# Kernel tuning notes

Hardware: AMD Instinct MI355X
Metric: run time of the kernel (lower is better)

## Reference

```python
import jax, jax.numpy as jnp
import numpy as np

N = 20000
E = 320000
IN_DIM, HID, MID, OUT, HEADS = 1536, 512, 128, 5, 8
NEG_SLOPE = 0.2
BN_EPS = 1e-5


def gat_conv(x, edge_index, W, a_src, a_dst, bias, heads, out_ch):
    """PyG-style GATConv (eval mode, self-loops already in edge_index).
    x: [N, F_in]; W: [F_in, heads*out_ch]; a_src/a_dst: [heads, out_ch]; bias: [heads*out_ch].
    Returns [N, heads*out_ch] (head concat)."""
    n = x.shape[0]
    h = (x @ W).reshape(n, heads, out_ch)              # [N,H,C]
    src, dst = edge_index[0], edge_index[1]
    al_s = jnp.sum(h * a_src, axis=-1)                 # [N,H]
    al_d = jnp.sum(h * a_dst, axis=-1)                 # [N,H]
    e = al_s[src] + al_d[dst]                          # [E,H]
    e = jnp.where(e >= 0, e, NEG_SLOPE * e)            # leaky_relu
    # segment softmax over incoming edges per dst node
    e_max = jax.ops.segment_max(e, dst, num_segments=n)
    e_max = jnp.where(jnp.isfinite(e_max), e_max, 0.0)
    ex = jnp.exp(e - e_max[dst])                       # [E,H]
    denom = jax.ops.segment_sum(ex, dst, num_segments=n)
    alpha = ex / (denom[dst] + 1e-16)                  # [E,H]
    msg = h[src] * alpha[:, :, None]                   # [E,H,C]
    out = jax.ops.segment_sum(msg, dst, num_segments=n)
    return out.reshape(n, heads * out_ch) + bias


def bn_eval(x, gamma, beta, mean, var):
    return (x - mean) * jax.lax.rsqrt(var + BN_EPS) * gamma + beta


def setup_inputs() -> dict:
    key = jax.random.key(0)
    ks = jax.random.split(key, 24)
    x = jax.random.normal(ks[0], (N, IN_DIM), dtype=jnp.float32)
    edge_index = jax.random.randint(ks[1], (2, E), 0, N, dtype=jnp.int32)

    def glorot(k, shape):
        fan = shape[0] + shape[-1]
        return jax.random.normal(k, shape, dtype=jnp.float32) * np.sqrt(2.0 / fan)

    inp = {"x": x, "edge_index": edge_index}
    # conv1: 1536 -> 8 heads x 64
    inp["W1"] = glorot(ks[2], (IN_DIM, HID))
    inp["as1"] = glorot(ks[3], (HEADS, HID // HEADS))
    inp["ad1"] = glorot(ks[4], (HEADS, HID // HEADS))
    inp["b1"] = jnp.zeros((HID,), jnp.float32)
    # conv2: 512 -> 8 heads x 16
    inp["W2"] = glorot(ks[5], (HID, MID))
    inp["as2"] = glorot(ks[6], (HEADS, MID // HEADS))
    inp["ad2"] = glorot(ks[7], (HEADS, MID // HEADS))
    inp["b2"] = jnp.zeros((MID,), jnp.float32)
    # conv3: 128 -> 1 head x 5
    inp["W3"] = glorot(ks[8], (MID, OUT))
    inp["as3"] = glorot(ks[9], (1, OUT))
    inp["ad3"] = glorot(ks[10], (1, OUT))
    inp["b3"] = jnp.zeros((OUT,), jnp.float32)
    # batchnorm params (eval mode, running stats)
    inp["g1"] = jax.random.normal(ks[11], (HID,), jnp.float32) * 0.1 + 1.0
    inp["be1"] = jax.random.normal(ks[12], (HID,), jnp.float32) * 0.1
    inp["m1"] = jax.random.normal(ks[13], (HID,), jnp.float32) * 0.1
    inp["v1"] = jax.random.uniform(ks[14], (HID,), jnp.float32, 0.5, 1.5)
    inp["g2"] = jax.random.normal(ks[15], (MID,), jnp.float32) * 0.1 + 1.0
    inp["be2"] = jax.random.normal(ks[16], (MID,), jnp.float32) * 0.1
    inp["m2"] = jax.random.normal(ks[17], (MID,), jnp.float32) * 0.1
    inp["v2"] = jax.random.uniform(ks[18], (MID,), jnp.float32, 0.5, 1.5)
    return inp


def reference(x, edge_index, W1, as1, ad1, b1, W2, as2, ad2, b2, W3, as3, ad3, b3,
              g1, be1, m1, v1, g2, be2, m2, v2):
    # add self-loops (PyG GATConv default)
    loops = jnp.arange(N, dtype=edge_index.dtype)
    ei = jnp.concatenate([edge_index, jnp.stack([loops, loops])], axis=1)

    h = jax.nn.relu(gat_conv(x, ei, W1, as1, ad1, b1, HEADS, HID // HEADS))
    h = bn_eval(h, g1, be1, m1, v1)
    h = jax.nn.relu(gat_conv(h, ei, W2, as2, ad2, b2, HEADS, MID // HEADS))
    h = bn_eval(h, g2, be2, m2, v2)
    h = gat_conv(h, ei, W3, as3, ad3, b3, 1, OUT)
    return jax.nn.log_softmax(h, axis=1)
```

## Files before the change

### kernel.cpp

```cpp
#include <hip/hip_runtime.h>
#include <math.h>

#define IN_DIM 1536
#define HID 512
#define MID 128
#define OUTC 5
#define HEADS 8
#define NEG_SLOPE 0.2f
#define BN_EPS 1e-5f

typedef __attribute__((ext_vector_type(8))) short s16x8;
typedef __attribute__((ext_vector_type(4))) float fx4;

__device__ __forceinline__ unsigned short bf16_rne(float f) {
    unsigned int u = __float_as_uint(f);
    u += 0x7fffu + ((u >> 16) & 1u);
    return (unsigned short)(u >> 16);
}
__device__ __forceinline__ float bf16_to_f32(unsigned short u) {
    return __uint_as_float((unsigned int)u << 16);
}

__device__ __forceinline__ void async_copy16(void* lds, const void* g) {
    __builtin_amdgcn_global_load_lds(
        (const __attribute__((address_space(1))) unsigned int*)g,
        (__attribute__((address_space(3))) unsigned int*)lds, 16, 0, 0);
}

__global__ void hist_kernel(const int* __restrict__ ei, int* __restrict__ deg,
                            int ET, int E) {
    int e = blockIdx.x * blockDim.x + threadIdx.x;
    if (e >= ET) return;
    int dst = (e < E) ? ei[E + e] : (e - E);
    atomicAdd(&deg[dst], 1);
}

__global__ __launch_bounds__(1024) void scan_kernel(const int* __restrict__ deg,
                                                    int* __restrict__ row_ptr,
                                                    int* __restrict__ cursor, int n) {
    __shared__ int partial[1024];
    int tid = threadIdx.x;
    int per = (n + 1023) / 1024;
    int base = tid * per;
    int s = 0;
    for (int i = 0; i < per; ++i) {
        int idx = base + i;
        if (idx < n) s += deg[idx];
    }
    partial[tid] = s;
    __syncthreads();
    for (int off = 1; off < 1024; off <<= 1) {
        int v = (tid >= off) ? partial[tid - off] : 0;
        __syncthreads();
        partial[tid] += v;
        __syncthreads();
    }
    int prefix = (tid == 0) ? 0 : partial[tid - 1];
    for (int i = 0; i < per; ++i) {
        int idx = base + i;
        if (idx < n) {
            row_ptr[idx] = prefix;
            cursor[idx] = prefix;
            prefix += deg[idx];
        }
    }
    if (tid == 1023) row_ptr[n] = partial[1023];
}

__global__ void scatter_kernel(const int* __restrict__ ei, int* __restrict__ cursor,
                               int* __restrict__ csr_src, int ET, int E) {
    int e = blockIdx.x * blockDim.x + threadIdx.x;
    if (e >= ET) return;
    int src, dst;
    if (e < E) { src = ei[e]; dst = ei[E + e]; }
    else       { src = dst = e - E; }
    int slot = atomicAdd(&cursor[dst], 1);
    csr_src[slot] = src;
}

__global__ void cvt_bf16_kernel(const float* __restrict__ in,
                                unsigned short* __restrict__ out, int n4) {
    int i = blockIdx.x * blockDim.x + threadIdx.x;
    if (i >= n4) return;
    float4 v = ((const float4*)in)[i];
    ushort4 o;
    o.x = bf16_rne(v.x); o.y = bf16_rne(v.y);
    o.z = bf16_rne(v.z); o.w = bf16_rne(v.w);
    ((ushort4*)out)[i] = o;
}

template <bool WLO>
__global__ __launch_bounds__(256) void transpose_split(
    const float* __restrict__ W, unsigned short* __restrict__ Th,
    unsigned short* __restrict__ Tl, int K, int Nn) {
    __shared__ float tile[32][33];
    int kb = blockIdx.y * 32, nb = blockIdx.x * 32;
    int tx = threadIdx.x & 31, ty = threadIdx.x >> 5;
#pragma unroll
    for (int r = 0; r < 4; ++r)
        tile[ty + r * 8][tx] = W[(size_t)(kb + ty + r * 8) * Nn + nb + tx];
    __syncthreads();
#pragma unroll
    for (int r = 0; r < 4; ++r) {
        int n = ty + r * 8;
        float v = tile[tx][n];
        unsigned short hi = bf16_rne(v);
        size_t o = (size_t)(nb + n) * K + kb + tx;
        Th[o] = hi;
        if (WLO) {
            float hif = __uint_as_float((unsigned int)hi << 16);
            Tl[o] = bf16_rne(v - hif);
        }
    }
}

__global__ __launch_bounds__(256) void gemm1_kernel(
    const unsigned short* __restrict__ A, const unsigned short* __restrict__ Bh,
    unsigned short* __restrict__ Cb, const float* __restrict__ a_s,
    const float* __restrict__ a_d, float* __restrict__ als,
    float* __restrict__ ald, int M, int N, int K, int MBLK) {
    int b = blockIdx.x;
    int xm = (b & 7) + 8 * (b >> 5);
    int ym = (b >> 3) & 3;
    if (xm >= MBLK) return;

    __shared__ unsigned short Asb[2][128 * 32];
    __shared__ unsigned short Bsb[2][128 * 32];

    const int tid = threadIdx.x;
    const int lane = tid & 63;
    const int wv = tid >> 6;
    const int row0 = xm * 128;
    const int nb0 = ym * 128;
    const int col = lane & 15;
    const int quad = lane >> 4;
    const int m0 = (wv >> 1) * 64;
    const int n0 = (wv & 1) * 64;

    const int s_row = lane >> 2;
    const int s_chunk = (lane & 3) ^ ((lane >> 3) & 3);
    int agr0 = row0 + (wv * 2 + 0) * 16 + s_row; if (agr0 >= M) agr0 = M - 1;
    int agr1 = row0 + (wv * 2 + 1) * 16 + s_row; if (agr1 >= M) agr1 = M - 1;
    const size_t ag0 = (size_t)agr0 * K + s_chunk * 8;
    const size_t ag1 = (size_t)agr1 * K + s_chunk * 8;
    const size_t bg0 = (size_t)(nb0 + (wv * 2 + 0) * 16 + s_row) * K + s_chunk * 8;
    const size_t bg1 = (size_t)(nb0 + (wv * 2 + 1) * 16 + s_row) * K + s_chunk * 8;

    const int rsw = (col >> 1) & 3;

    fx4 acc[4][4];
#pragma unroll
    for (int i = 0; i < 4; ++i)
#pragma unroll
        for (int j = 0; j < 4; ++j) acc[i][j] = (fx4){0.f, 0.f, 0.f, 0.f};

    async_copy16(&Asb[0][(wv * 2 + 0) * 512], A + ag0);
    async_copy16(&Asb[0][(wv * 2 + 1) * 512], A + ag1);
    async_copy16(&Bsb[0][(wv * 2 + 0) * 512], Bh + bg0);
    async_copy16(&Bsb[0][(wv * 2 + 1) * 512], Bh + bg1);
    __syncthreads();

    int cur = 0;
    for (int k0 = 0; k0 < K; k0 += 32) {
        const int nxt = cur ^ 1;
        if (k0 + 32 < K) {
            const int kn = k0 + 32;
            async_copy16(&Asb[nxt][(wv * 2 + 0) * 512], A + ag0 + kn);
            async_copy16(&Asb[nxt][(wv * 2 + 1) * 512], A + ag1 + kn);
            async_copy16(&Bsb[nxt][(wv * 2 + 0) * 512], Bh + bg0 + kn);
            async_copy16(&Bsb[nxt][(wv * 2 + 1) * 512], Bh + bg1 + kn);
        }
        s16x8 afr[4], bfr[4];
#pragma unroll
        for (int i = 0; i < 4; ++i)
            afr[i] = *(const s16x8*)&Asb[cur][(m0 + i * 16 + col) * 32 + (quad ^ rsw) * 8];
#pragma unroll
        for (int j = 0; j < 4; ++j)
            bfr[j] = *(const s16x8*)&Bsb[cur][(n0 + j * 16 + col) * 32 + (quad ^ rsw) * 8];
#pragma unroll
        for (int i = 0; i < 4; ++i)
#pragma unroll
            for (int j = 0; j < 4; ++j)
                acc[i][j] = __builtin_amdgcn_mfma_f32_16x16x32_bf16(afr[i], bfr[j], acc[i][j], 0, 0, 0);
        __syncthreads();
        cur = nxt;
    }

#pragma unroll
    for (int i = 0; i < 4; ++i) {
        int gr0 = row0 + m0 + i * 16 + quad * 4;
#pragma unroll
        for (int j = 0; j < 4; ++j) {
            int gc = nb0 + n0 + j * 16 + col;
#pragma unroll
            for (int r = 0; r < 4; ++r) {
                int gr = gr0 + r;
                if (gr < M) Cb[(size_t)gr * N + gc] = bf16_rne(acc[i][j][r]);
            }
        }
    }

    const int head = (nb0 + n0) >> 6;
    float asv[4], adv[4];
#pragma unroll
    for (int j = 0; j < 4; ++j) {
        asv[j] = a_s[head * 64 + j * 16 + col];
        adv[j] = a_d[head * 64 + j * 16 + col];
    }
#pragma unroll
    for (int i = 0; i < 4; ++i) {
#pragma unroll
        for (int r = 0; r < 4; ++r) {
            float ss = acc[i][0][r] * asv[0] + acc[i][1][r] * asv[1] +
                       acc[i][2][r] * asv[2] + acc[i][3][r] * asv[3];
            float sd = acc[i][0][r] * adv[0] + acc[i][1][r] * adv[1] +
                       acc[i][2][r] * adv[2] + acc[i][3][r] * adv[3];
#pragma unroll
            for (int off = 8; off; off >>= 1) {
                ss += __shfl_xor(ss, off);
                sd += __shfl_xor(sd, off);
            }
            if (col == 0) {
                int gr = row0 + m0 + i * 16 + quad * 4 + r;
                if (gr < M) {
                    als[gr * HEADS + head] = ss;
                    ald[gr * HEADS + head] = sd;
                }
            }
        }
    }
}

__global__ __launch_bounds__(256) void gemm2_kernel(
    const unsigned short* __restrict__ A, const unsigned short* __restrict__ Bh,
    const unsigned short* __restrict__ Bl, unsigned short* __restrict__ Cb,
    const float* __restrict__ a_s, const float* __restrict__ a_d,
    float* __restrict__ als, float* __restrict__ ald, int M, int N, int K) {
    __shared__ unsigned short Asb[2][32 * 32];
    __shared__ unsigned short Bhb[2][128 * 32];
    __shared__ unsigned short Blb[2][128 * 32];

    const int tid = threadIdx.x;
    const int lane = tid & 63;
    const int wv = tid >> 6;
    const int row0 = blockIdx.x * 32;
    const int col = lane & 15;
    const int quad = lane >> 4;
    const int m0 = (wv >> 1) * 16;
    const int n0 = (wv & 1) * 64;
    const int b_row = lane >> 2;
    const int b_chunk = (lane & 3) ^ ((lane >> 3) & 3);
    const int rsw = (col >> 1) & 3;

    const int t0 = wv * 2, t1 = t0 + 1;
    const size_t bgo0 = (size_t)(t0 * 16 + b_row) * K + b_chunk * 8;
    const size_t bgo1 = (size_t)(t1 * 16 + b_row) * K + b_chunk * 8;
    int agr = row0 + wv * 16 + b_row; if (agr >= M) agr = M - 1;
    const size_t ago = (size_t)agr * K + b_chunk * 8;

    fx4 acc[4];
#pragma unroll
    for (int j = 0; j < 4; ++j) acc[j] = (fx4){0.f, 0.f, 0.f, 0.f};

    auto stage = [&](int buf, int k) {
        async_copy16(&Bhb[buf][t0 * 512], Bh + bgo0 + k);
        async_copy16(&Bhb[buf][t1 * 512], Bh + bgo1 + k);
        async_copy16(&Blb[buf][t0 * 512], Bl + bgo0 + k);
        async_copy16(&Blb[buf][t1 * 512], Bl + bgo1 + k);
        if (wv < 2) async_copy16(&Asb[buf][wv * 512], A + ago + k);
    };

    stage(0, 0);
    __syncthreads();

    int cur = 0;
    for (int k0 = 0; k0 < K; k0 += 32) {
        const int nxt = cur ^ 1;
        if (k0 + 32 < K) stage(nxt, k0 + 32);
        s16x8 a, bh4[4], bl4[4];
        a = *(const s16x8*)&Asb[cur][(m0 + col) * 32 + (quad ^ rsw) * 8];
#pragma unroll
        for (int j = 0; j < 4; ++j) {
            int rb = (n0 + j * 16 + col) * 32 + (quad ^ rsw) * 8;
            bh4[j] = *(const s16x8*)&Bhb[cur][rb];
            bl4[j] = *(const s16x8*)&Blb[cur][rb];
        }
#pragma unroll
        for (int j = 0; j < 4; ++j) {
            acc[j] = __builtin_amdgcn_mfma_f32_16x16x32_bf16(a, bl4[j], acc[j], 0, 0, 0);
            acc[j] = __builtin_amdgcn_mfma_f32_16x16x32_bf16(a, bh4[j], acc[j], 0, 0, 0);
        }
        __syncthreads();
        cur = nxt;
    }

    int gr0 = row0 + m0 + quad * 4;
#pragma unroll
    for (int j = 0; j < 4; ++j) {
        int gc = n0 + j * 16 + col;
#pragma unroll
        for (int r = 0; r < 4; ++r) {
            int gr = gr0 + r;
            if (gr < M) Cb[(size_t)gr * N + gc] = bf16_rne(acc[j][r]);
        }
    }

    float asv[4], adv[4];
#pragma unroll
    for (int j = 0; j < 4; ++j) {
        asv[j] = a_s[n0 + j * 16 + col];
        adv[j] = a_d[n0 + j * 16 + col];
    }
#pragma unroll
    for (int j = 0; j < 4; ++j) {
        int head = (n0 >> 4) + j;
#pragma unroll
        for (int r = 0; r < 4; ++r) {
            float ss = acc[j][r] * asv[j];
            float sd = acc[j][r] * adv[j];
#pragma unroll
            for (int off = 8; off; off >>= 1) {
                ss += __shfl_xor(ss, off);
                sd += __shfl_xor(sd, off);
            }
            if (col == 0) {
                int gr = gr0 + r;
                if (gr < M) {
                    als[gr * HEADS + head] = ss;
                    ald[gr * HEADS + head] = sd;
                }
            }
        }
    }
}

template <int F, int VEC>
__global__ __launch_bounds__(128) void agg_fused_kernel(
    const unsigned short* __restrict__ hlin, const float* __restrict__ als,
    const float* __restrict__ ald, const int* __restrict__ row_ptr,
    const int* __restrict__ csr_src, const float* __restrict__ bias,
    const float* __restrict__ gamma, const float* __restrict__ beta,
    const float* __restrict__ mean, const float* __restrict__ var,
    unsigned short* __restrict__ outh) {
    int dst = blockIdx.x;
    int tid = threadIdx.x;
    int f0 = tid * VEC;
    int h = tid >> 4;
    __shared__ float exs[16][8];
    __shared__ int srcs[16];
    int s0 = row_ptr[dst], s1 = row_ptr[dst + 1];
    int cj = tid >> 3, ch = tid & 7;
    float ald_c = ald[dst * HEADS + ch];
    float acc[VEC];
#pragma unroll
    for (int v = 0; v < VEC; ++v) acc[v] = 0.f;
    float den = 0.f;

    for (int base = s0; base < s1; base += 16) {
        int take = min(16, s1 - base);
        if (cj < take) {
            int src = csr_src[base + cj];
            if (ch == 0) srcs[cj] = src;
            float e = als[src * HEADS + ch] + ald_c;
            e = (e >= 0.f) ? e : NEG_SLOPE * e;
            exs[cj][ch] = __expf(e);
        }
        __syncthreads();
        for (int jj = 0; jj < take; ++jj) {
            int src = srcs[jj];
            float a = exs[jj][h];
            den += a;
            const unsigned short* rp = &hlin[(size_t)src * F + f0];
            ushort4 u = *(const ushort4*)rp;
            acc[0] += a * bf16_to_f32(u.x);
            acc[1] += a * bf16_to_f32(u.y);
            acc[2] += a * bf16_to_f32(u.z);
            acc[3] += a * bf16_to_f32(u.w);
        }
        __syncthreads();
    }

    float rd = 1.f / (den + 1e-16f);
    ushort4 o;
    unsigned short* op = (unsigned short*)&o;
#pragma unroll
    for (int v = 0; v < VEC; ++v) {
        int f = f0 + v;
        float val = acc[v] * rd + bias[f];
        val = fmaxf(val, 0.f);
        val = (val - mean[f]) * rsqrtf(var[f] + BN_EPS) * gamma[f] + beta[f];
        op[v] = bf16_rne(val);
    }
    *(ushort4*)&outh[(size_t)dst * F + f0] = o;
}

__global__ __launch_bounds__(128) void agg2_l3_kernel(
    const unsigned short* __restrict__ hlin, const float* __restrict__ als,
    const float* __restrict__ ald, const int* __restrict__ row_ptr,
    const int* __restrict__ csr_src, const float* __restrict__ bias,
    const float* __restrict__ gamma, const float* __restrict__ beta,
    const float* __restrict__ mean, const float* __restrict__ var,
    const float* __restrict__ W3, const float* __restrict__ as3,
    const float* __restrict__ ad3, float* __restrict__ h3lin,
    float* __restrict__ als3, float* __restrict__ ald3) {
    int dst = blockIdx.x;
    int tid = threadIdx.x;
    int h = tid >> 4;
    __shared__ float exs[16][8];
    __shared__ int srcs[16];
    __shared__ float red[2][OUTC];
    int s0 = row_ptr[dst], s1 = row_ptr[dst + 1];
    int cj = tid >> 3, ch = tid & 7;
    float ald_c = ald[dst * HEADS + ch];
    float acc = 0.f, den = 0.f;

    for (int base = s0; base < s1; base += 16) {
        int take = min(16, s1 - base);
        if (cj < take) {
            int src = csr_src[base + cj];
            if (ch == 0) srcs[cj] = src;
            float e = als[src * HEADS + ch] + ald_c;
            e = (e >= 0.f) ? e : NEG_SLOPE * e;
            exs[cj][ch] = __expf(e);
        }
        __syncthreads();
        for (int jj = 0; jj < take; ++jj) {
            int src = srcs[jj];
            float a = exs[jj][h];
            den += a;
            acc += a * bf16_to_f32(hlin[(size_t)src * MID + tid]);
        }
        __syncthreads();
    }

    float val = acc / (den + 1e-16f) + bias[tid];
    val = fmaxf(val, 0.f);
    val = (val - mean[tid]) * rsqrtf(var[tid] + BN_EPS) * gamma[tid] + beta[tid];

    float p[OUTC];
#pragma unroll
    for (int c = 0; c < OUTC; ++c) p[c] = val * W3[tid * OUTC + c];
#pragma unroll
    for (int off = 32; off; off >>= 1) {
#pragma unroll
        for (int c = 0; c < OUTC; ++c) p[c] += __shfl_xor(p[c], off);
    }
    int wv = tid >> 6;
    if ((tid & 63) == 0) {
#pragma unroll
        for (int c = 0; c < OUTC; ++c) red[wv][c] = p[c];
    }
    __syncthreads();
    if (tid == 0) {
        float ss = 0.f, sd = 0.f;
#pragma unroll
        for (int c = 0; c < OUTC; ++c) {
            float v = red[0][c] + red[1][c];
            h3lin[(size_t)dst * OUTC + c] = v;
            ss += v * as3[c];
            sd += v * ad3[c];
        }
        als3[dst] = ss;
        ald3[dst] = sd;
    }
}

__global__ __launch_bounds__(256) void agg3_lsm_kernel(
    const float* __restrict__ h3lin, const float* __restrict__ als,
    const float* __restrict__ ald, const int* __restrict__ row_ptr,
    const int* __restrict__ csr_src, const float* __restrict__ b3,
    float* __restrict__ out, int n) {
    int g = blockIdx.x * blockDim.x + threadIdx.x;
    int dst = g >> 4;
    int l = g & 15;
    if (dst >= n) return;
    int s0 = row_ptr[dst], s1 = row_ptr[dst + 1];
    float ad = ald[dst];
    float den = 0.f;
    float acc[OUTC] = {0.f, 0.f, 0.f, 0.f, 0.f};
    for (int j = s0 + l; j < s1; j += 16) {
        int src = csr_src[j];
        float e = als[src] + ad;
        e = (e >= 0.f) ? e : NEG_SLOPE * e;
        float x = __expf(e);
        den += x;
        const float* hp = h3lin + (size_t)src * OUTC;
#pragma unroll
        for (int c = 0; c < OUTC; ++c) acc[c] += x * hp[c];
    }
#pragma unroll
    for (int off = 8; off; off >>= 1) {
        den += __shfl_xor(den, off);
#pragma unroll
        for (int c = 0; c < OUTC; ++c) acc[c] += __shfl_xor(acc[c], off);
    }
    if (l == 0) {
        float rd = 1.f / (den + 1e-16f);
        float m = -INFINITY;
#pragma unroll
        for (int c = 0; c < OUTC; ++c) {
            acc[c] = acc[c] * rd + b3[c];
            m = fmaxf(m, acc[c]);
        }
        float s = 0.f;
#pragma unroll
        for (int c = 0; c < OUTC; ++c) s += __expf(acc[c] - m);
        float lse = m + __logf(s);
#pragma unroll
        for (int c = 0; c < OUTC; ++c) out[(size_t)dst * OUTC + c] = acc[c] - lse;
    }
}

extern "C" void kernel_launch(void* const* d_in, const int* in_sizes, int n_in,
                              void* d_out, int out_size, void* d_ws, size_t ws_size,
                              hipStream_t stream) {
    const float* x   = (const float*)d_in[0];
    const int*   ei  = (const int*)d_in[1];
    const float* W1  = (const float*)d_in[2];
    const float* as1 = (const float*)d_in[3];
    const float* ad1 = (const float*)d_in[4];
    const float* b1  = (const float*)d_in[5];
    const float* W2  = (const float*)d_in[6];
    const float* as2 = (const float*)d_in[7];
    const float* ad2 = (const float*)d_in[8];
    const float* b2  = (const float*)d_in[9];
    const float* W3  = (const float*)d_in[10];
    const float* as3 = (const float*)d_in[11];
    const float* ad3 = (const float*)d_in[12];
    const float* b3  = (const float*)d_in[13];
    const float* g1  = (const float*)d_in[14];
    const float* be1 = (const float*)d_in[15];
    const float* m1  = (const float*)d_in[16];
    const float* v1  = (const float*)d_in[17];
    const float* g2  = (const float*)d_in[18];
    const float* be2 = (const float*)d_in[19];
    const float* m2  = (const float*)d_in[20];
    const float* v2  = (const float*)d_in[21];

    const int N = in_sizes[0] / IN_DIM;
    const int E = in_sizes[1] / 2;
    const int ET = E + N;
    const int MBLK1 = (N + 127) / 128;
    const int MBLK2 = (N + 31) / 32;

    char* ws = (char*)d_ws;
    size_t off = 0;
    auto take = [&](size_t bytes) -> char* {
        char* p = ws + off;
        off += (bytes + 255) & ~(size_t)255;
        return p;
    };
    int* deg      = (int*)take((size_t)N * 4);
    int* row_ptr  = (int*)take((size_t)(N + 1) * 4);
    int* cursor   = (int*)take((size_t)N * 4);
    int* csr_src  = (int*)take((size_t)ET * 4);
    unsigned short* W1h = (unsigned short*)take((size_t)HID * IN_DIM * 2);
    unsigned short* W2h = (unsigned short*)take((size_t)MID * HID * 2);
    unsigned short* W2l = (unsigned short*)take((size_t)MID * HID * 2);
    unsigned short* xh  = (unsigned short*)take((size_t)N * IN_DIM * 2);
    unsigned short* h1lin = (unsigned short*)take((size_t)N * HID * 2);
    unsigned short* h1h   = (unsigned short*)take((size_t)N * HID * 2);
    unsigned short* h2lin = (unsigned short*)take((size_t)N * MID * 2);
    float* h3lin  = (float*)take((size_t)N * OUTC * 4);
    float* als    = (float*)take((size_t)N * HEADS * 4);
    float* ald    = (float*)take((size_t)N * HEADS * 4);
    float* als3   = (float*)take((size_t)N * 4);
    float* ald3   = (float*)take((size_t)N * 4);

    hipMemsetAsync(deg, 0, (size_t)N * 4, stream);
    hist_kernel<<<(ET + 255) / 256, 256, 0, stream>>>(ei, deg, ET, E);
    scan_kernel<<<1, 1024, 0, stream>>>(deg, row_ptr, cursor, N);
    scatter_kernel<<<(ET + 255) / 256, 256, 0, stream>>>(ei, cursor, csr_src, ET, E);
    transpose_split<false><<<dim3(HID / 32, IN_DIM / 32), 256, 0, stream>>>(
        W1, W1h, nullptr, IN_DIM, HID);
    transpose_split<true><<<dim3(MID / 32, HID / 32), 256, 0, stream>>>(
        W2, W2h, W2l, HID, MID);
    {
        int n4 = N * IN_DIM / 4;
        cvt_bf16_kernel<<<(n4 + 255) / 256, 256, 0, stream>>>(x, xh, n4);
    }

    gemm1_kernel<<<640, 256, 0, stream>>>(xh, W1h, h1lin, as1, ad1, als, ald,
                                          N, HID, IN_DIM, MBLK1);
    agg_fused_kernel<HID, 4><<<N, 128, 0, stream>>>(
        h1lin, als, ald, row_ptr, csr_src, b1, g1, be1, m1, v1, h1h);

    gemm2_kernel<<<MBLK2, 256, 0, stream>>>(h1h, W2h, W2l, h2lin, as2, ad2,
                                            als, ald, N, MID, HID);
    agg2_l3_kernel<<<N, 128, 0, stream>>>(
        h2lin, als, ald, row_ptr, csr_src, b2, g2, be2, m2, v2,
        W3, as3, ad3, h3lin, als3, ald3);

    agg3_lsm_kernel<<<(N * 16 + 255) / 256, 256, 0, stream>>>(
        h3lin, als3, ald3, row_ptr, csr_src, b3, (float*)d_out, N);
}
```

Measured before the change: 446.0 us.

## Fuse fp32-to-bf16 conversion of x into gemm1 tile loads and merge transposes

Removes the standalone conversion kernel and the bf16 copy of x. gemm1 now loads fp32 rows of x into registers, converts them, and writes the bf16 tile to LDS after the MFMA work for software pipelining. The two weight transpose launches are merged into one kernel. The trade is losing async LDS copies for A and having each N-block reread fp32 data, which doubles the per-tile read bytes.

Measured after the change: 474.1 us. +6.3%, slower.

```diff
diff --git a/kernel.cpp b/kernel.cpp
--- a/kernel.cpp
+++ b/kernel.cpp
@@ -25,6 +25,15 @@
     __builtin_amdgcn_global_load_lds(
         (const __attribute__((address_space(1))) unsigned int*)g,
         (__attribute__((address_space(3))) unsigned int*)lds, 16, 0, 0);
+}
+
+__device__ __forceinline__ void store_bf16x8(unsigned short* p, float4 a, float4 b) {
+    union { s16x8 v; unsigned short u[8]; } o;
+    o.u[0] = bf16_rne(a.x); o.u[1] = bf16_rne(a.y);
+    o.u[2] = bf16_rne(a.z); o.u[3] = bf16_rne(a.w);
+    o.u[4] = bf16_rne(b.x); o.u[5] = bf16_rne(b.y);
+    o.u[6] = bf16_rne(b.z); o.u[7] = bf16_rne(b.w);
+    *(s16x8*)p = o.v;
 }
 
 __global__ void hist_kernel(const int* __restrict__ ei, int* __restrict__ deg,
@@ -78,23 +87,24 @@
     csr_src[slot] = src;
 }
 
-__global__ void cvt_bf16_kernel(const float* __restrict__ in,
-                                unsigned short* __restrict__ out, int n4) {
-    int i = blockIdx.x * blockDim.x + threadIdx.x;
-    if (i >= n4) return;
-    float4 v = ((const float4*)in)[i];
-    ushort4 o;
-    o.x = bf16_rne(v.x); o.y = bf16_rne(v.y);
-    o.z = bf16_rne(v.z); o.w = bf16_rne(v.w);
-    ((ushort4*)out)[i] = o;
-}
-
-template <bool WLO>
-__global__ __launch_bounds__(256) void transpose_split(
-    const float* __restrict__ W, unsigned short* __restrict__ Th,
-    unsigned short* __restrict__ Tl, int K, int Nn) {
+__global__ __launch_bounds__(256) void transpose_both_kernel(
+    const float* __restrict__ W1, unsigned short* __restrict__ W1h,
+    const float* __restrict__ W2, unsigned short* __restrict__ W2h,
+    unsigned short* __restrict__ W2l) {
     __shared__ float tile[32][33];
-    int kb = blockIdx.y * 32, nb = blockIdx.x * 32;
+    int b = blockIdx.x;
+    const float* W;
+    unsigned short *Th, *Tl;
+    int K, Nn, kb, nb;
+    bool wlo;
+    if (b < 768) {
+        W = W1; Th = W1h; Tl = nullptr; wlo = false; K = IN_DIM; Nn = HID;
+        nb = (b & 15) * 32; kb = (b >> 4) * 32;
+    } else {
+        int b2 = b - 768;
+        W = W2; Th = W2h; Tl = W2l; wlo = true; K = HID; Nn = MID;
+        nb = (b2 & 3) * 32; kb = (b2 >> 2) * 32;
+    }
     int tx = threadIdx.x & 31, ty = threadIdx.x >> 5;
 #pragma unroll
     for (int r = 0; r < 4; ++r)
@@ -107,7 +117,7 @@
         unsigned short hi = bf16_rne(v);
         size_t o = (size_t)(nb + n) * K + kb + tx;
         Th[o] = hi;
-        if (WLO) {
+        if (wlo) {
             float hif = __uint_as_float((unsigned int)hi << 16);
             Tl[o] = bf16_rne(v - hif);
         }
@@ -115,7 +125,7 @@
 }
 
 __global__ __launch_bounds__(256) void gemm1_kernel(
-    const unsigned short* __restrict__ A, const unsigned short* __restrict__ Bh,
+    const float* __restrict__ Af, const unsigned short* __restrict__ Bh,
     unsigned short* __restrict__ Cb, const float* __restrict__ a_s,
     const float* __restrict__ a_d, float* __restrict__ als,
     float* __restrict__ ald, int M, int N, int K, int MBLK) {
@@ -137,12 +147,18 @@
     const int m0 = (wv >> 1) * 64;
     const int n0 = (wv & 1) * 64;
 
+    const int ar0 = tid >> 2;
+    const int ac = tid & 3;
+    const int ag = ac ^ ((ar0 >> 1) & 3);
+    int arow0 = row0 + ar0;      if (arow0 >= M) arow0 = M - 1;
+    int arow1 = row0 + ar0 + 64; if (arow1 >= M) arow1 = M - 1;
+    const size_t aoff0 = (size_t)arow0 * K + ag * 8;
+    const size_t aoff1 = (size_t)arow1 * K + ag * 8;
+    const int lds_a0 = ar0 * 32 + ac * 8;
+    const int lds_a1 = (ar0 + 64) * 32 + ac * 8;
+
     const int s_row = lane >> 2;
     const int s_chunk = (lane & 3) ^ ((lane >> 3) & 3);
-    int agr0 = row0 + (wv * 2 + 0) * 16 + s_row; if (agr0 >= M) agr0 = M - 1;
-    int agr1 = row0 + (wv * 2 + 1) * 16 + s_row; if (agr1 >= M) agr1 = M - 1;
-    const size_t ag0 = (size_t)agr0 * K + s_chunk * 8;
-    const size_t ag1 = (size_t)agr1 * K + s_chunk * 8;
     const size_t bg0 = (size_t)(nb0 + (wv * 2 + 0) * 16 + s_row) * K + s_chunk * 8;
     const size_t bg1 = (size_t)(nb0 + (wv * 2 + 1) * 16 + s_row) * K + s_chunk * 8;
 
@@ -154,19 +170,29 @@
 #pragma unroll
         for (int j = 0; j < 4; ++j) acc[i][j] = (fx4){0.f, 0.f, 0.f, 0.f};
 
-    async_copy16(&Asb[0][(wv * 2 + 0) * 512], A + ag0);
-    async_copy16(&Asb[0][(wv * 2 + 1) * 512], A + ag1);
-    async_copy16(&Bsb[0][(wv * 2 + 0) * 512], Bh + bg0);
-    async_copy16(&Bsb[0][(wv * 2 + 1) * 512], Bh + bg1);
+    {
+        float4 p00 = *(const float4*)(Af + aoff0);
+        float4 p01 = *(const float4*)(Af + aoff0 + 4);
+        float4 p10 = *(const float4*)(Af + aoff1);
+        float4 p11 = *(const float4*)(Af + aoff1 + 4);
+        async_copy16(&Bsb[0][(wv * 2 + 0) * 512], Bh + bg0);
+        async_copy16(&Bsb[0][(wv * 2 + 1) * 512], Bh + bg1);
+        store_bf16x8(&Asb[0][lds_a0], p00, p01);
+        store_bf16x8(&Asb[0][lds_a1], p10, p11);
+    }
     __syncthreads();
 
     int cur = 0;
     for (int k0 = 0; k0 < K; k0 += 32) {
         const int nxt = cur ^ 1;
-        if (k0 + 32 < K) {
+        const bool more = (k0 + 32 < K);
+        float4 p00, p01, p10, p11;
+        if (more) {
             const int kn = k0 + 32;
-            async_copy16(&Asb[nxt][(wv * 2 + 0) * 512], A + ag0 + kn);
-            async_copy16(&Asb[nxt][(wv * 2 + 1) * 512], A + ag1 + kn);
+            p00 = *(const float4*)(Af + aoff0 + kn);
+            p01 = *(const float4*)(Af + aoff0 + kn + 4);
+            p10 = *(const float4*)(Af + aoff1 + kn);
+            p11 = *(const float4*)(Af + aoff1 + kn + 4);
             async_copy16(&Bsb[nxt][(wv * 2 + 0) * 512], Bh + bg0 + kn);
             async_copy16(&Bsb[nxt][(wv * 2 + 1) * 512], Bh + bg1 + kn);
         }
@@ -182,6 +208,10 @@
 #pragma unroll
             for (int j = 0; j < 4; ++j)
                 acc[i][j] = __builtin_amdgcn_mfma_f32_16x16x32_bf16(afr[i], bfr[j], acc[i][j], 0, 0, 0);
+        if (more) {
+            store_bf16x8(&Asb[nxt][lds_a0], p00, p01);
+            store_bf16x8(&Asb[nxt][lds_a1], p10, p11);
+        }
         __syncthreads();
         cur = nxt;
     }
@@ -557,7 +587,6 @@
     unsigned short* W1h = (unsigned short*)take((size_t)HID * IN_DIM * 2);
     unsigned short* W2h = (unsigned short*)take((size_t)MID * HID * 2);
     unsigned short* W2l = (unsigned short*)take((size_t)MID * HID * 2);
-    unsigned short* xh  = (unsigned short*)take((size_t)N * IN_DIM * 2);
     unsigned short* h1lin = (unsigned short*)take((size_t)N * HID * 2);
     unsigned short* h1h   = (unsigned short*)take((size_t)N * HID * 2);
     unsigned short* h2lin = (unsigned short*)take((size_t)N * MID * 2);
@@ -571,16 +600,9 @@
     hist_kernel<<<(ET + 255) / 256, 256, 0, stream>>>(ei, deg, ET, E);
     scan_kernel<<<1, 1024, 0, stream>>>(deg, row_ptr, cursor, N);
     scatter_kernel<<<(ET + 255) / 256, 256, 0, stream>>>(ei, cursor, csr_src, ET, E);
-    transpose_split<false><<<dim3(HID / 32, IN_DIM / 32), 256, 0, stream>>>(
-        W1, W1h, nullptr, IN_DIM, HID);
-    transpose_split<true><<<dim3(MID / 32, HID / 32), 256, 0, stream>>>(
-        W2, W2h, W2l, HID, MID);
-    {
-        int n4 = N * IN_DIM / 4;
-        cvt_bf16_kernel<<<(n4 + 255) / 256, 256, 0, stream>>>(x, xh, n4);
-    }
-
-    gemm1_kernel<<<640, 256, 0, stream>>>(xh, W1h, h1lin, as1, ad1, als, ald,
+    transpose_both_kernel<<<832, 256, 0, stream>>>(W1, W1h, W2, W2h, W2l);
+
+    gemm1_kernel<<<640, 256, 0, stream>>>(x, W1h, h1lin, as1, ad1, als, ald,
                                           N, HID, IN_DIM, MBLK1);
     agg_fused_kernel<HID, 4><<<N, 128, 0, stream>>>(
         h1lin, als, ald, row_ptr, csr_src, b1, g1, be1, m1, v1, h1h);
```

## Use one wavefront per node in layer-1 aggregation and merge weight transposes

Applied to the files above, without the earlier changes.

Layer-1 aggregation now runs one 64-lane wavefront per destination node with four nodes per block. Attention weights and source indices are passed between lanes with shuffles, so the shared memory and block barriers are gone. Each lane loads 8 bf16 features at once in a single 16-byte access. The two weight-transpose launches are merged into one kernel to save a launch, at the cost of handling only 8 edges per chunk instead of 16.

Result: no change. 446.7 us (+0.2%).

```diff
diff --git a/kernel.cpp b/kernel.cpp
--- a/kernel.cpp
+++ b/kernel.cpp
@@ -89,12 +89,24 @@
     ((ushort4*)out)[i] = o;
 }
 
-template <bool WLO>
-__global__ __launch_bounds__(256) void transpose_split(
-    const float* __restrict__ W, unsigned short* __restrict__ Th,
-    unsigned short* __restrict__ Tl, int K, int Nn) {
+__global__ __launch_bounds__(256) void transpose_both_kernel(
+    const float* __restrict__ W1, unsigned short* __restrict__ W1h,
+    const float* __restrict__ W2, unsigned short* __restrict__ W2h,
+    unsigned short* __restrict__ W2l) {
     __shared__ float tile[32][33];
-    int kb = blockIdx.y * 32, nb = blockIdx.x * 32;
+    int b = blockIdx.x;
+    const float* W;
+    unsigned short *Th, *Tl;
+    int K, Nn, kb, nb;
+    bool wlo;
+    if (b < 768) {
+        W = W1; Th = W1h; Tl = nullptr; wlo = false; K = IN_DIM; Nn = HID;
+        nb = (b & 15) * 32; kb = (b >> 4) * 32;
+    } else {
+        int b2 = b - 768;
+        W = W2; Th = W2h; Tl = W2l; wlo = true; K = HID; Nn = MID;
+        nb = (b2 & 3) * 32; kb = (b2 >> 2) * 32;
+    }
     int tx = threadIdx.x & 31, ty = threadIdx.x >> 5;
 #pragma unroll
     for (int r = 0; r < 4; ++r)
@@ -107,7 +119,7 @@
         unsigned short hi = bf16_rne(v);
         size_t o = (size_t)(nb + n) * K + kb + tx;
         Th[o] = hi;
-        if (WLO) {
+        if (wlo) {
             float hif = __uint_as_float((unsigned int)hi << 16);
             Tl[o] = bf16_rne(v - hif);
         }
@@ -334,64 +346,60 @@
     }
 }
 
-template <int F, int VEC>
-__global__ __launch_bounds__(128) void agg_fused_kernel(
+__global__ __launch_bounds__(256) void agg1_wave_kernel(
     const unsigned short* __restrict__ hlin, const float* __restrict__ als,
     const float* __restrict__ ald, const int* __restrict__ row_ptr,
     const int* __restrict__ csr_src, const float* __restrict__ bias,
     const float* __restrict__ gamma, const float* __restrict__ beta,
     const float* __restrict__ mean, const float* __restrict__ var,
-    unsigned short* __restrict__ outh) {
-    int dst = blockIdx.x;
-    int tid = threadIdx.x;
-    int f0 = tid * VEC;
-    int h = tid >> 4;
-    __shared__ float exs[16][8];
-    __shared__ int srcs[16];
+    unsigned short* __restrict__ outh, int n) {
+    int lane = threadIdx.x & 63;
+    int dst = blockIdx.x * 4 + (threadIdx.x >> 6);
+    if (dst >= n) return;
+    const int f0 = lane * 8;
+    const int h = lane >> 3;
+    const int j8 = lane >> 3;
+    const int ch = lane & 7;
+    float ald_c = ald[dst * HEADS + ch];
+
     int s0 = row_ptr[dst], s1 = row_ptr[dst + 1];
-    int cj = tid >> 3, ch = tid & 7;
-    float ald_c = ald[dst * HEADS + ch];
-    float acc[VEC];
-#pragma unroll
-    for (int v = 0; v < VEC; ++v) acc[v] = 0.f;
+    float acc[8];
+#pragma unroll
+    for (int v = 0; v < 8; ++v) acc[v] = 0.f;
     float den = 0.f;
 
-    for (int base = s0; base < s1; base += 16) {
-        int take = min(16, s1 - base);
-        if (cj < take) {
-            int src = csr_src[base + cj];
-            if (ch == 0) srcs[cj] = src;
-            float e = als[src * HEADS + ch] + ald_c;
+    for (int base = s0; base < s1; base += 8) {
+        int take = min(8, s1 - base);
+        float ex = 0.f;
+        int src_l = 0;
+        if (j8 < take) {
+            src_l = csr_src[base + j8];
+            float e = als[src_l * HEADS + ch] + ald_c;
             e = (e >= 0.f) ? e : NEG_SLOPE * e;
-            exs[cj][ch] = __expf(e);
-        }
-        __syncthreads();
+            ex = __expf(e);
+        }
         for (int jj = 0; jj < take; ++jj) {
-            int src = srcs[jj];
-            float a = exs[jj][h];
+            int src = __shfl(src_l, jj * 8);
+            float a = __shfl(ex, jj * 8 + h);
             den += a;
-            const unsigned short* rp = &hlin[(size_t)src * F + f0];
-            ushort4 u = *(const ushort4*)rp;
-            acc[0] += a * bf16_to_f32(u.x);
-            acc[1] += a * bf16_to_f32(u.y);
-            acc[2] += a * bf16_to_f32(u.z);
-            acc[3] += a * bf16_to_f32(u.w);
-        }
-        __syncthreads();
+            union { s16x8 v; unsigned short u[8]; } w;
+            w.v = *(const s16x8*)&hlin[(size_t)src * HID + f0];
+#pragma unroll
+            for (int v = 0; v < 8; ++v) acc[v] += a * bf16_to_f32(w.u[v]);
+        }
     }
 
     float rd = 1.f / (den + 1e-16f);
-    ushort4 o;
-    unsigned short* op = (unsigned short*)&o;
-#pragma unroll
-    for (int v = 0; v < VEC; ++v) {
+    union { s16x8 v; unsigned short u[8]; } o;
+#pragma unroll
+    for (int v = 0; v < 8; ++v) {
         int f = f0 + v;
         float val = acc[v] * rd + bias[f];
         val = fmaxf(val, 0.f);
         val = (val - mean[f]) * rsqrtf(var[f] + BN_EPS) * gamma[f] + beta[f];
-        op[v] = bf16_rne(val);
-    }
-    *(ushort4*)&outh[(size_t)dst * F + f0] = o;
+        o.u[v] = bf16_rne(val);
+    }
+    *(s16x8*)&outh[(size_t)dst * HID + f0] = o.v;
 }
 
 __global__ __launch_bounds__(128) void agg2_l3_kernel(
@@ -571,10 +579,7 @@
     hist_kernel<<<(ET + 255) / 256, 256, 0, stream>>>(ei, deg, ET, E);
     scan_kernel<<<1, 1024, 0, stream>>>(deg, row_ptr, cursor, N);
     scatter_kernel<<<(ET + 255) / 256, 256, 0, stream>>>(ei, cursor, csr_src, ET, E);
-    transpose_split<false><<<dim3(HID / 32, IN_DIM / 32), 256, 0, stream>>>(
-        W1, W1h, nullptr, IN_DIM, HID);
-    transpose_split<true><<<dim3(MID / 32, HID / 32), 256, 0, stream>>>(
-        W2, W2h, W2l, HID, MID);
+    transpose_both_kernel<<<832, 256, 0, stream>>>(W1, W1h, W2, W2h, W2l);
     {
         int n4 = N * IN_DIM / 4;
         cvt_bf16_kernel<<<(n4 + 255) / 256, 256, 0, stream>>>(x, xh, n4);
@@ -582,8 +587,8 @@
 
     gemm1_kernel<<<640, 256, 0, stream>>>(xh, W1h, h1lin, as1, ad1, als, ald,
                                           N, HID, IN_DIM, MBLK1);
-    agg_fused_kernel<HID, 4><<<N, 128, 0, stream>>>(
-        h1lin, als, ald, row_ptr, csr_src, b1, g1, be1, m1, v1, h1h);
+    agg1_wave_kernel<<<(N + 3) / 4, 256, 0, stream>>>(
+        h1lin, als, ald, row_ptr, csr_src, b1, g1, be1, m1, v1, h1h, N);
 
     gemm2_kernel<<<MBLK2, 256, 0, stream>>>(h1h, W2h, W2l, h2lin, as2, ad2,
                                             als, ald, N, MID, HID);
```
